# Optimization experiments

Hardware: AMD Instinct MI355X
Metric: run time of the kernel (lower is better)

Reference implementation:

```python
import jax, jax.numpy as jnp
import numpy as np

B, T, Q, K, H = 8, 128, 64, 64, 4  # batch, agents, q_dim, kv_dim, heads; neighbors n = T-1


def setup_inputs() -> dict:
    key = jax.random.key(0)
    ks = jax.random.split(key, 9)
    s = 0.05
    return {
        "q_x": jax.random.normal(ks[0], (B, T, Q), dtype=jnp.float32),
        "kv_x": jax.random.normal(ks[1], (B, T, T - 1, K), dtype=jnp.float32),
        # nn.Linear weights stored (out_features, in_features), y = x @ W.T + b
        "Wk": jax.random.normal(ks[2], (H * K, K), dtype=jnp.float32) * s,      # tokeys (no bias)
        "Wq": jax.random.normal(ks[3], (H * K, Q), dtype=jnp.float32) * s,      # toqueries (no bias)
        "Wv": jax.random.normal(ks[4], (H * K, K + Q), dtype=jnp.float32) * s,  # tovalues
        "bv": jax.random.normal(ks[5], (H * K,), dtype=jnp.float32) * s,
        "bias": jax.random.uniform(ks[6], (K,), dtype=jnp.float32, minval=-0.1, maxval=0.1),
        "ws": jax.random.normal(ks[7], (K,), dtype=jnp.float32) * s,            # score_proj weight (1, K) -> (K,)
        "bs": jax.random.normal(ks[8], (), dtype=jnp.float32) * s,              # score_proj bias
    }


def reference(q_x, kv_x, Wk, Wq, Wv, bv, bias, ws, bs):
    b, t, n, k = kv_x.shape            # n = t - 1 neighbors
    q = q_x.shape[-1]
    h = Wk.shape[0] // k
    # key / query projections
    keys = jnp.einsum('btnk,ok->btno', kv_x, Wk).reshape(b, t, n, h, k)
    queries = jnp.einsum('btq,oq->bto', q_x, Wq).reshape(b, t, 1, h, k)
    # additive (Bahdanau) score: linear(tanh(keys + queries + bias)) -> scalar per (b,t,n,h)
    score = jnp.einsum('btnhk,k->btnh', jnp.tanh(keys + queries + bias), ws) + bs
    # values from concat(kv, broadcast query features)
    q_exp = jnp.broadcast_to(q_x[:, :, None, :], (b, t, n, q))
    value_input = jnp.concatenate([kv_x, q_exp], axis=-1)      # (b,t,n,k+q)
    values = (jnp.einsum('btnc,oc->btno', value_input, Wv) + bv).reshape(b, t, n, h, k)
    # softmax over neighbors, weighted sum of values
    w = jax.nn.softmax(score, axis=2)                          # (b,t,n,h)
    x = jnp.einsum('btnh,btnhk->bthk', w, values).reshape(b, t, h * k)
    return x
```

## Files before the change

kernel.cpp:

```cpp
#include <hip/hip_runtime.h>
#include <hip/hip_bf16.h>

#define NB 127
#define SCALE 2.885390081777927f

typedef __attribute__((ext_vector_type(8))) short bf16x8;
typedef __attribute__((ext_vector_type(4))) float f32x4;

#define WKP_S  0
#define WVP_S  16384
#define WQP_S  32768
#define WVQP_S 49152
#define WS_NEEDED ((size_t)(4 * 16384 * 2))

__device__ __forceinline__ short bfs(float f) {
  __hip_bfloat16 h = __float2bfloat16(f);
  return __builtin_bit_cast(short, h);
}
__device__ __forceinline__ unsigned packbf2(float a, float b) {
  unsigned lo = (unsigned short)bfs(a);
  unsigned hi = (unsigned short)bfs(b);
  return lo | (hi << 16);
}
__device__ __forceinline__ float b2f(short s) {
  unsigned u = ((unsigned)(unsigned short)s) << 16;
  return __builtin_bit_cast(float, u);
}
__device__ __forceinline__ bf16x8 gath_s(const float* __restrict__ p, float s) {
  float4 a = *(const float4*)p;
  float4 b = *(const float4*)(p + 4);
  bf16x8 f;
  f[0] = bfs(a.x * s); f[1] = bfs(a.y * s); f[2] = bfs(a.z * s); f[3] = bfs(a.w * s);
  f[4] = bfs(b.x * s); f[5] = bfs(b.y * s); f[6] = bfs(b.z * s); f[7] = bfs(b.w * s);
  return f;
}

__global__ __launch_bounds__(256, 2) void
pack_kernel(const float* __restrict__ Wk, const float* __restrict__ Wq,
            const float* __restrict__ Wv, short* __restrict__ dstall)
{
  const int blk = blockIdx.x;
  const int tid = threadIdx.x;
  const int m = blk >> 4, sub = blk & 15;
  const float* src; int stride, off, dsto; float scl;
  if (m == 0)      { src = Wk; stride = 64;  off = 0;  dsto = WKP_S;  scl = SCALE; }
  else if (m == 1) { src = Wv; stride = 128; off = 0;  dsto = WVP_S;  scl = 1.f; }
  else if (m == 2) { src = Wq; stride = 64;  off = 0;  dsto = WQP_S;  scl = SCALE; }
  else             { src = Wv; stride = 128; off = 64; dsto = WVQP_S; scl = 1.f; }
  short* dst = dstall + dsto;
  int i4 = sub * 256 + tid;
  int o = i4 >> 4, c4 = i4 & 15;
  float4 v = ((const float4*)(src + o * stride + off))[c4];
  int k0 = c4 * 4;
  int kt = k0 >> 5, gg = (k0 & 31) >> 3, j0 = k0 & 7;
  int head = o >> 6, nt = (o >> 4) & 3, ol = o & 15;
  int di = ((((head * 4 + nt) * 2 + kt) * 64) + gg * 16 + ol) * 8 + j0;
  *(uint2*)(dst + di) = make_uint2(packbf2(v.x * scl, v.y * scl),
                                   packbf2(v.z * scl, v.w * scl));
}

template <int PREP>
__global__ __launch_bounds__(256, 4) void
rnn_attn_kernel(const float* __restrict__ q_x, const float* __restrict__ kv_x,
                const float* __restrict__ Wk, const float* __restrict__ Wq,
                const float* __restrict__ Wv, const float* __restrict__ bv,
                const float* __restrict__ bias, const float* __restrict__ wsc,
                const short* __restrict__ pack, float* __restrict__ out)
{
  __shared__ __align__(16) unsigned char Atile[128 * 128];
  __shared__ float scs[4][128];
  __shared__ float4 qv_lds[4][4][4];

  const int tid = threadIdx.x;
  const int bt = blockIdx.x;
  const int lane = tid & 63;
  const int head = tid >> 6;
  const int l15 = lane & 15;
  const int g = lane >> 4;

  const float* kv = kv_x + (size_t)bt * (NB * 64);
  #pragma unroll
  for (int i = 0; i < 8; ++i) {
    int idx = i * 256 + tid;
    int row = idx >> 4, c = idx & 15;
    float4 v = (row < NB) ? ((const float4*)kv)[idx] : make_float4(0.f, 0.f, 0.f, 0.f);
    int byte = (row << 7) + (c << 3);
    byte ^= ((row & 7) << 4);
    *(uint2*)(&Atile[byte]) = make_uint2(packbf2(v.x, v.y), packbf2(v.z, v.w));
  }

  f32x4 qq[4];
  {
    bf16x8 qf0 = gath_s(q_x + bt * 64 + g * 8, 1.f);
    bf16x8 qf1 = gath_s(q_x + bt * 64 + 32 + g * 8, 1.f);
    #pragma unroll
    for (int nt = 0; nt < 4; ++nt) {
      bf16x8 wv0, wv1;
      if (PREP) {
        const bf16x8* pv = (const bf16x8*)(pack + WVQP_S);
        wv0 = pv[((head * 4 + nt) * 2 + 0) * 64 + lane];
        wv1 = pv[((head * 4 + nt) * 2 + 1) * 64 + lane];
      } else {
        int o = head * 64 + nt * 16 + l15;
        wv0 = gath_s(Wv + o * 128 + 64 + g * 8, 1.f);
        wv1 = gath_s(Wv + o * 128 + 64 + 32 + g * 8, 1.f);
      }
      float4 bv4 = ((const float4*)(bv + head * 64))[nt * 4 + g];
      f32x4 b = (f32x4){bv4.x, bv4.y, bv4.z, bv4.w};
      b = __builtin_amdgcn_mfma_f32_16x16x32_bf16(wv0, qf0, b, 0, 0, 0);
      b = __builtin_amdgcn_mfma_f32_16x16x32_bf16(wv1, qf1, b, 0, 0, 0);
      if (l15 == 0) qv_lds[head][nt][g] = make_float4(b[0], b[1], b[2], b[3]);
    }
    #pragma unroll
    for (int nt = 0; nt < 4; ++nt) {
      bf16x8 wq0, wq1;
      if (PREP) {
        const bf16x8* pw = (const bf16x8*)(pack + WQP_S);
        wq0 = pw[((head * 4 + nt) * 2 + 0) * 64 + lane];
        wq1 = pw[((head * 4 + nt) * 2 + 1) * 64 + lane];
      } else {
        int o = head * 64 + nt * 16 + l15;
        wq0 = gath_s(Wq + o * 64 + g * 8, SCALE);
        wq1 = gath_s(Wq + o * 64 + 32 + g * 8, SCALE);
      }
      float4 bs4 = ((const float4*)bias)[nt * 4 + g];
      f32x4 a = (f32x4){bs4.x * SCALE, bs4.y * SCALE, bs4.z * SCALE, bs4.w * SCALE};
      a = __builtin_amdgcn_mfma_f32_16x16x32_bf16(wq0, qf0, a, 0, 0, 0);
      a = __builtin_amdgcn_mfma_f32_16x16x32_bf16(wq1, qf1, a, 0, 0, 0);
      qq[nt] = a;
    }
  }

  __syncthreads();

  #pragma unroll
  for (int h = 0; h < 2; ++h) {
    bf16x8 b00, b01, b10, b11;
    if (PREP) {
      const bf16x8* pw = (const bf16x8*)(pack + WKP_S);
      b00 = pw[((head * 4 + 2 * h + 0) * 2 + 0) * 64 + lane];
      b01 = pw[((head * 4 + 2 * h + 0) * 2 + 1) * 64 + lane];
      b10 = pw[((head * 4 + 2 * h + 1) * 2 + 0) * 64 + lane];
      b11 = pw[((head * 4 + 2 * h + 1) * 2 + 1) * 64 + lane];
    } else {
      int o0 = head * 64 + (2 * h) * 16 + l15;
      b00 = gath_s(Wk + o0 * 64 + g * 8, SCALE);
      b01 = gath_s(Wk + o0 * 64 + 32 + g * 8, SCALE);
      b10 = gath_s(Wk + (o0 + 16) * 64 + g * 8, SCALE);
      b11 = gath_s(Wk + (o0 + 16) * 64 + 32 + g * 8, SCALE);
    }
    float4 ta = ((const float4*)wsc)[(2 * h) * 4 + g];
    float4 tb = ((const float4*)wsc)[(2 * h + 1) * 4 + g];
    f32x4 wsa = (f32x4){-2.f * ta.x, -2.f * ta.y, -2.f * ta.z, -2.f * ta.w};
    f32x4 wsb = (f32x4){-2.f * tb.x, -2.f * tb.y, -2.f * tb.z, -2.f * tb.w};
    f32x4 qa = qq[2 * h], qb = qq[2 * h + 1];

    #pragma unroll 1
    for (int mt = 0; mt < 8; ++mt) {
      int row = mt * 16 + l15;
      int byte0 = (row << 7) + g * 16;
      int swz = (l15 & 7) << 4;
      bf16x8 a0 = *(const bf16x8*)(&Atile[byte0 ^ swz]);
      bf16x8 a1 = *(const bf16x8*)(&Atile[(byte0 + 64) ^ swz]);
      float p = 0.f;
      f32x4 acc = qa;
      acc = __builtin_amdgcn_mfma_f32_16x16x32_bf16(b00, a0, acc, 0, 0, 0);
      acc = __builtin_amdgcn_mfma_f32_16x16x32_bf16(b01, a1, acc, 0, 0, 0);
      #pragma unroll
      for (int r = 0; r < 4; ++r)
        p = fmaf(wsa[r], __builtin_amdgcn_rcpf(__builtin_amdgcn_exp2f(acc[r]) + 1.f), p);
      f32x4 acc2 = qb;
      acc2 = __builtin_amdgcn_mfma_f32_16x16x32_bf16(b10, a0, acc2, 0, 0, 0);
      acc2 = __builtin_amdgcn_mfma_f32_16x16x32_bf16(b11, a1, acc2, 0, 0, 0);
      #pragma unroll
      for (int r = 0; r < 4; ++r)
        p = fmaf(wsb[r], __builtin_amdgcn_rcpf(__builtin_amdgcn_exp2f(acc2[r]) + 1.f), p);
      p += __shfl_xor(p, 16);
      p += __shfl_xor(p, 32);
      if (g == 0) {
        int idx = mt * 16 + l15;
        scs[head][idx] = h ? (scs[head][idx] + p) : p;
      }
    }
  }

  {
    float s0 = scs[head][l15 + 0],  s1 = scs[head][l15 + 16];
    float s2 = scs[head][l15 + 32], s3 = scs[head][l15 + 48];
    float s4 = scs[head][l15 + 64], s5 = scs[head][l15 + 80];
    float s6 = scs[head][l15 + 96], s7 = scs[head][l15 + 112];
    if (l15 == 15) s7 = -3.0e38f;
    float m = fmaxf(fmaxf(fmaxf(s0, s1), fmaxf(s2, s3)),
                    fmaxf(fmaxf(s4, s5), fmaxf(s6, s7)));
    #pragma unroll
    for (int d = 1; d < 16; d <<= 1) m = fmaxf(m, __shfl_xor(m, d));
    float e0 = __expf(s0 - m), e1 = __expf(s1 - m), e2 = __expf(s2 - m), e3 = __expf(s3 - m);
    float e4 = __expf(s4 - m), e5 = __expf(s5 - m), e6 = __expf(s6 - m), e7 = __expf(s7 - m);
    float sum = ((e0 + e1) + (e2 + e3)) + ((e4 + e5) + (e6 + e7));
    #pragma unroll
    for (int d = 1; d < 16; d <<= 1) sum += __shfl_xor(sum, d);
    float inv = __builtin_amdgcn_rcpf(sum);
    if (g == 0) {
      scs[head][l15 + 0]  = e0 * inv; scs[head][l15 + 16] = e1 * inv;
      scs[head][l15 + 32] = e2 * inv; scs[head][l15 + 48] = e3 * inv;
      scs[head][l15 + 64] = e4 * inv; scs[head][l15 + 80] = e5 * inv;
      scs[head][l15 + 96] = e6 * inv; scs[head][l15 + 112] = e7 * inv;
    }
  }

  float pvp0[8], pvp1[8];
  #pragma unroll
  for (int j = 0; j < 8; ++j) { pvp0[j] = 0.f; pvp1[j] = 0.f; }
  #pragma unroll 1
  for (int mt = 0; mt < 8; ++mt) {
    int row = mt * 16 + l15;
    int byte0 = (row << 7) + g * 16;
    int swz = (l15 & 7) << 4;
    bf16x8 a0 = *(const bf16x8*)(&Atile[byte0 ^ swz]);
    bf16x8 a1 = *(const bf16x8*)(&Atile[(byte0 + 64) ^ swz]);
    float w = scs[head][mt * 16 + l15];
    #pragma unroll
    for (int j = 0; j < 8; ++j) {
      pvp0[j] = fmaf(w, b2f(a0[j]), pvp0[j]);
      pvp1[j] = fmaf(w, b2f(a1[j]), pvp1[j]);
    }
  }
  bf16x8 pa0, pa1;
  #pragma unroll
  for (int j = 0; j < 8; ++j) { pa0[j] = bfs(pvp0[j]); pa1[j] = bfs(pvp1[j]); }

  float tt[4];
  #pragma unroll 2
  for (int nt = 0; nt < 4; ++nt) {
    bf16x8 bw0, bw1;
    if (PREP) {
      const bf16x8* pw = (const bf16x8*)(pack + WVP_S);
      bw0 = pw[((head * 4 + nt) * 2 + 0) * 64 + lane];
      bw1 = pw[((head * 4 + nt) * 2 + 1) * 64 + lane];
    } else {
      int o = head * 64 + nt * 16 + l15;
      bw0 = gath_s(Wv + o * 128 + g * 8, 1.f);
      bw1 = gath_s(Wv + o * 128 + 32 + g * 8, 1.f);
    }
    f32x4 c = (f32x4){0.f, 0.f, 0.f, 0.f};
    c = __builtin_amdgcn_mfma_f32_16x16x32_bf16(pa0, bw0, c, 0, 0, 0);
    c = __builtin_amdgcn_mfma_f32_16x16x32_bf16(pa1, bw1, c, 0, 0, 0);
    float t = (c[0] + c[1]) + (c[2] + c[3]);
    t += __shfl_xor(t, 16);
    t += __shfl_xor(t, 32);
    tt[nt] = t;
  }

  float v = tt[0];
  v = (g == 1) ? tt[1] : v;
  v = (g == 2) ? tt[2] : v;
  v = (g == 3) ? tt[3] : v;
  float qv = ((const float*)&qv_lds[head][g][l15 >> 2])[l15 & 3];
  out[bt * 256 + head * 64 + lane] = v + qv;
}

extern "C" void kernel_launch(void* const* d_in, const int* in_sizes, int n_in,
                              void* d_out, int out_size, void* d_ws, size_t ws_size,
                              hipStream_t stream) {
  const float* q_x  = (const float*)d_in[0];
  const float* kv_x = (const float*)d_in[1];
  const float* Wk   = (const float*)d_in[2];
  const float* Wq   = (const float*)d_in[3];
  const float* Wv   = (const float*)d_in[4];
  const float* bv   = (const float*)d_in[5];
  const float* bias = (const float*)d_in[6];
  const float* wsc  = (const float*)d_in[7];
  float* out = (float*)d_out;
  short* pack = (short*)d_ws;

  if (ws_size >= WS_NEEDED) {
    pack_kernel<<<64, 256, 0, stream>>>(Wk, Wq, Wv, pack);
    rnn_attn_kernel<1><<<1024, 256, 0, stream>>>(q_x, kv_x, Wk, Wq, Wv, bv, bias, wsc, pack, out);
  } else {
    rnn_attn_kernel<0><<<1024, 256, 0, stream>>>(q_x, kv_x, Wk, Wq, Wv, bv, bias, wsc, pack, out);
  }
}
```

Before: 29.07 us.

## Process two (b,t) rows per block with a double-size kv tile

Each block now loads the kv tiles for two consecutive (b,t) rows into a doubled shared-memory buffer up front, then processes the two rows sequentially, and the grid is halved. The goal is more outstanding global loads per block and amortised block launch and setup cost. In exchange, LDS use per block roughly doubles, which lowers occupancy, and the second row's compute no longer overlaps with another block's loads. The scs and qv_lds buffers are reused across the two rows with no barrier between them. That is safe only because each wave touches only its own head slice.

```diff
diff --git a/kernel.cpp b/kernel.cpp
--- a/kernel.cpp
+++ b/kernel.cpp
@@ -67,196 +67,202 @@
                 const float* __restrict__ bias, const float* __restrict__ wsc,
                 const short* __restrict__ pack, float* __restrict__ out)
 {
-  __shared__ __align__(16) unsigned char Atile[128 * 128];
+  __shared__ __align__(16) unsigned char Atile[2][128 * 128];
   __shared__ float scs[4][128];
   __shared__ float4 qv_lds[4][4][4];
 
   const int tid = threadIdx.x;
-  const int bt = blockIdx.x;
+  const int bt0 = blockIdx.x * 2;
   const int lane = tid & 63;
   const int head = tid >> 6;
   const int l15 = lane & 15;
   const int g = lane >> 4;
 
-  const float* kv = kv_x + (size_t)bt * (NB * 64);
   #pragma unroll
-  for (int i = 0; i < 8; ++i) {
+  for (int i = 0; i < 16; ++i) {
     int idx = i * 256 + tid;
-    int row = idx >> 4, c = idx & 15;
-    float4 v = (row < NB) ? ((const float4*)kv)[idx] : make_float4(0.f, 0.f, 0.f, 0.f);
-    int byte = (row << 7) + (c << 3);
-    byte ^= ((row & 7) << 4);
-    *(uint2*)(&Atile[byte]) = make_uint2(packbf2(v.x, v.y), packbf2(v.z, v.w));
+    int tb = idx >> 11;
+    int id2 = idx & 2047;
+    int row = id2 >> 4, c = id2 & 15;
+    const float* kv = kv_x + (size_t)(bt0 + tb) * (NB * 64);
+    float4 v = (row < NB) ? ((const float4*)kv)[id2] : make_float4(0.f, 0.f, 0.f, 0.f);
+    int byte = (tb << 14) + ((((row << 7) + (c << 3))) ^ ((row & 7) << 4));
+    *(uint2*)(&Atile[0][0] + byte) = make_uint2(packbf2(v.x, v.y), packbf2(v.z, v.w));
   }
-
-  f32x4 qq[4];
-  {
-    bf16x8 qf0 = gath_s(q_x + bt * 64 + g * 8, 1.f);
-    bf16x8 qf1 = gath_s(q_x + bt * 64 + 32 + g * 8, 1.f);
+  __syncthreads();
+
+  #pragma unroll 1
+  for (int b = 0; b < 2; ++b) {
+    const int bt = bt0 + b;
+    const int tbase = b << 14;
+
+    f32x4 qq[4];
+    {
+      bf16x8 qf0 = gath_s(q_x + bt * 64 + g * 8, 1.f);
+      bf16x8 qf1 = gath_s(q_x + bt * 64 + 32 + g * 8, 1.f);
+      #pragma unroll
+      for (int nt = 0; nt < 4; ++nt) {
+        bf16x8 wv0, wv1;
+        if (PREP) {
+          const bf16x8* pv = (const bf16x8*)(pack + WVQP_S);
+          wv0 = pv[((head * 4 + nt) * 2 + 0) * 64 + lane];
+          wv1 = pv[((head * 4 + nt) * 2 + 1) * 64 + lane];
+        } else {
+          int o = head * 64 + nt * 16 + l15;
+          wv0 = gath_s(Wv + o * 128 + 64 + g * 8, 1.f);
+          wv1 = gath_s(Wv + o * 128 + 64 + 32 + g * 8, 1.f);
+        }
+        float4 bv4 = ((const float4*)(bv + head * 64))[nt * 4 + g];
+        f32x4 bb = (f32x4){bv4.x, bv4.y, bv4.z, bv4.w};
+        bb = __builtin_amdgcn_mfma_f32_16x16x32_bf16(wv0, qf0, bb, 0, 0, 0);
+        bb = __builtin_amdgcn_mfma_f32_16x16x32_bf16(wv1, qf1, bb, 0, 0, 0);
+        if (l15 == 0) qv_lds[head][nt][g] = make_float4(bb[0], bb[1], bb[2], bb[3]);
+      }
+      #pragma unroll
+      for (int nt = 0; nt < 4; ++nt) {
+        bf16x8 wq0, wq1;
+        if (PREP) {
+          const bf16x8* pw = (const bf16x8*)(pack + WQP_S);
+          wq0 = pw[((head * 4 + nt) * 2 + 0) * 64 + lane];
+          wq1 = pw[((head * 4 + nt) * 2 + 1) * 64 + lane];
+        } else {
+          int o = head * 64 + nt * 16 + l15;
+          wq0 = gath_s(Wq + o * 64 + g * 8, SCALE);
+          wq1 = gath_s(Wq + o * 64 + 32 + g * 8, SCALE);
+        }
+        float4 bs4 = ((const float4*)bias)[nt * 4 + g];
+        f32x4 a = (f32x4){bs4.x * SCALE, bs4.y * SCALE, bs4.z * SCALE, bs4.w * SCALE};
+        a = __builtin_amdgcn_mfma_f32_16x16x32_bf16(wq0, qf0, a, 0, 0, 0);
+        a = __builtin_amdgcn_mfma_f32_16x16x32_bf16(wq1, qf1, a, 0, 0, 0);
+        qq[nt] = a;
+      }
+    }
+
     #pragma unroll
-    for (int nt = 0; nt < 4; ++nt) {
-      bf16x8 wv0, wv1;
+    for (int h = 0; h < 2; ++h) {
+      bf16x8 b00, b01, b10, b11;
       if (PREP) {
-        const bf16x8* pv = (const bf16x8*)(pack + WVQP_S);
-        wv0 = pv[((head * 4 + nt) * 2 + 0) * 64 + lane];
-        wv1 = pv[((head * 4 + nt) * 2 + 1) * 64 + lane];
+        const bf16x8* pw = (const bf16x8*)(pack + WKP_S);
+        b00 = pw[((head * 4 + 2 * h + 0) * 2 + 0) * 64 + lane];
+        b01 = pw[((head * 4 + 2 * h + 0) * 2 + 1) * 64 + lane];
+        b10 = pw[((head * 4 + 2 * h + 1) * 2 + 0) * 64 + lane];
+        b11 = pw[((head * 4 + 2 * h + 1) * 2 + 1) * 64 + lane];
       } else {
-        int o = head * 64 + nt * 16 + l15;
-        wv0 = gath_s(Wv + o * 128 + 64 + g * 8, 1.f);
-        wv1 = gath_s(Wv + o * 128 + 64 + 32 + g * 8, 1.f);
-      }
-      float4 bv4 = ((const float4*)(bv + head * 64))[nt * 4 + g];
-      f32x4 b = (f32x4){bv4.x, bv4.y, bv4.z, bv4.w};
-      b = __builtin_amdgcn_mfma_f32_16x16x32_bf16(wv0, qf0, b, 0, 0, 0);
-      b = __builtin_amdgcn_mfma_f32_16x16x32_bf16(wv1, qf1, b, 0, 0, 0);
-      if (l15 == 0) qv_lds[head][nt][g] = make_float4(b[0], b[1], b[2], b[3]);
-    }
+        int o0 = head * 64 + (2 * h) * 16 + l15;
+        b00 = gath_s(Wk + o0 * 64 + g * 8, SCALE);
+        b01 = gath_s(Wk + o0 * 64 + 32 + g * 8, SCALE);
+        b10 = gath_s(Wk + (o0 + 16) * 64 + g * 8, SCALE);
+        b11 = gath_s(Wk + (o0 + 16) * 64 + 32 + g * 8, SCALE);
+      }
+      float4 ta = ((const float4*)wsc)[(2 * h) * 4 + g];
+      float4 tb = ((const float4*)wsc)[(2 * h + 1) * 4 + g];
+      f32x4 wsa = (f32x4){-2.f * ta.x, -2.f * ta.y, -2.f * ta.z, -2.f * ta.w};
+      f32x4 wsb = (f32x4){-2.f * tb.x, -2.f * tb.y, -2.f * tb.z, -2.f * tb.w};
+      f32x4 qa = qq[2 * h], qb = qq[2 * h + 1];
+
+      #pragma unroll 1
+      for (int mt = 0; mt < 8; ++mt) {
+        int row = mt * 16 + l15;
+        int byte0 = tbase + (row << 7) + g * 16;
+        int swz = (l15 & 7) << 4;
+        bf16x8 a0 = *(const bf16x8*)(&Atile[0][0] + (byte0 ^ swz));
+        bf16x8 a1 = *(const bf16x8*)(&Atile[0][0] + ((byte0 + 64) ^ swz));
+        float p = 0.f;
+        f32x4 acc = qa;
+        acc = __builtin_amdgcn_mfma_f32_16x16x32_bf16(b00, a0, acc, 0, 0, 0);
+        acc = __builtin_amdgcn_mfma_f32_16x16x32_bf16(b01, a1, acc, 0, 0, 0);
+        #pragma unroll
+        for (int r = 0; r < 4; ++r)
+          p = fmaf(wsa[r], __builtin_amdgcn_rcpf(__builtin_amdgcn_exp2f(acc[r]) + 1.f), p);
+        f32x4 acc2 = qb;
+        acc2 = __builtin_amdgcn_mfma_f32_16x16x32_bf16(b10, a0, acc2, 0, 0, 0);
+        acc2 = __builtin_amdgcn_mfma_f32_16x16x32_bf16(b11, a1, acc2, 0, 0, 0);
+        #pragma unroll
+        for (int r = 0; r < 4; ++r)
+          p = fmaf(wsb[r], __builtin_amdgcn_rcpf(__builtin_amdgcn_exp2f(acc2[r]) + 1.f), p);
+        p += __shfl_xor(p, 16);
+        p += __shfl_xor(p, 32);
+        if (g == 0) {
+          int idx = mt * 16 + l15;
+          scs[head][idx] = h ? (scs[head][idx] + p) : p;
+        }
+      }
+    }
+
+    {
+      float s0 = scs[head][l15 + 0],  s1 = scs[head][l15 + 16];
+      float s2 = scs[head][l15 + 32], s3 = scs[head][l15 + 48];
+      float s4 = scs[head][l15 + 64], s5 = scs[head][l15 + 80];
+      float s6 = scs[head][l15 + 96], s7 = scs[head][l15 + 112];
+      if (l15 == 15) s7 = -3.0e38f;
+      float m = fmaxf(fmaxf(fmaxf(s0, s1), fmaxf(s2, s3)),
+                      fmaxf(fmaxf(s4, s5), fmaxf(s6, s7)));
+      #pragma unroll
+      for (int d = 1; d < 16; d <<= 1) m = fmaxf(m, __shfl_xor(m, d));
+      float e0 = __expf(s0 - m), e1 = __expf(s1 - m), e2 = __expf(s2 - m), e3 = __expf(s3 - m);
+      float e4 = __expf(s4 - m), e5 = __expf(s5 - m), e6 = __expf(s6 - m), e7 = __expf(s7 - m);
+      float sum = ((e0 + e1) + (e2 + e3)) + ((e4 + e5) + (e6 + e7));
+      #pragma unroll
+      for (int d = 1; d < 16; d <<= 1) sum += __shfl_xor(sum, d);
+      float inv = __builtin_amdgcn_rcpf(sum);
+      if (g == 0) {
+        scs[head][l15 + 0]  = e0 * inv; scs[head][l15 + 16] = e1 * inv;
+        scs[head][l15 + 32] = e2 * inv; scs[head][l15 + 48] = e3 * inv;
+        scs[head][l15 + 64] = e4 * inv; scs[head][l15 + 80] = e5 * inv;
+        scs[head][l15 + 96] = e6 * inv; scs[head][l15 + 112] = e7 * inv;
+      }
+    }
+
+    float pvp0[8], pvp1[8];
     #pragma unroll
-    for (int nt = 0; nt < 4; ++nt) {
-      bf16x8 wq0, wq1;
-      if (PREP) {
-        const bf16x8* pw = (const bf16x8*)(pack + WQP_S);
-        wq0 = pw[((head * 4 + nt) * 2 + 0) * 64 + lane];
-        wq1 = pw[((head * 4 + nt) * 2 + 1) * 64 + lane];
-      } else {
-        int o = head * 64 + nt * 16 + l15;
-        wq0 = gath_s(Wq + o * 64 + g * 8, SCALE);
-        wq1 = gath_s(Wq + o * 64 + 32 + g * 8, SCALE);
-      }
-      float4 bs4 = ((const float4*)bias)[nt * 4 + g];
-      f32x4 a = (f32x4){bs4.x * SCALE, bs4.y * SCALE, bs4.z * SCALE, bs4.w * SCALE};
-      a = __builtin_amdgcn_mfma_f32_16x16x32_bf16(wq0, qf0, a, 0, 0, 0);
-      a = __builtin_amdgcn_mfma_f32_16x16x32_bf16(wq1, qf1, a, 0, 0, 0);
-      qq[nt] = a;
-    }
-  }
-
-  __syncthreads();
-
-  #pragma unroll
-  for (int h = 0; h < 2; ++h) {
-    bf16x8 b00, b01, b10, b11;
-    if (PREP) {
-      const bf16x8* pw = (const bf16x8*)(pack + WKP_S);
-      b00 = pw[((head * 4 + 2 * h + 0) * 2 + 0) * 64 + lane];
-      b01 = pw[((head * 4 + 2 * h + 0) * 2 + 1) * 64 + lane];
-      b10 = pw[((head * 4 + 2 * h + 1) * 2 + 0) * 64 + lane];
-      b11 = pw[((head * 4 + 2 * h + 1) * 2 + 1) * 64 + lane];
-    } else {
-      int o0 = head * 64 + (2 * h) * 16 + l15;
-      b00 = gath_s(Wk + o0 * 64 + g * 8, SCALE);
-      b01 = gath_s(Wk + o0 * 64 + 32 + g * 8, SCALE);
-      b10 = gath_s(Wk + (o0 + 16) * 64 + g * 8, SCALE);
-      b11 = gath_s(Wk + (o0 + 16) * 64 + 32 + g * 8, SCALE);
-    }
-    float4 ta = ((const float4*)wsc)[(2 * h) * 4 + g];
-    float4 tb = ((const float4*)wsc)[(2 * h + 1) * 4 + g];
-    f32x4 wsa = (f32x4){-2.f * ta.x, -2.f * ta.y, -2.f * ta.z, -2.f * ta.w};
-    f32x4 wsb = (f32x4){-2.f * tb.x, -2.f * tb.y, -2.f * tb.z, -2.f * tb.w};
-    f32x4 qa = qq[2 * h], qb = qq[2 * h + 1];
-
+    for (int j = 0; j < 8; ++j) { pvp0[j] = 0.f; pvp1[j] = 0.f; }
     #pragma unroll 1
     for (int mt = 0; mt < 8; ++mt) {
       int row = mt * 16 + l15;
-      int byte0 = (row << 7) + g * 16;
+      int byte0 = tbase + (row << 7) + g * 16;
       int swz = (l15 & 7) << 4;
-      bf16x8 a0 = *(const bf16x8*)(&Atile[byte0 ^ swz]);
-      bf16x8 a1 = *(const bf16x8*)(&Atile[(byte0 + 64) ^ swz]);
-      float p = 0.f;
-      f32x4 acc = qa;
-      acc = __builtin_amdgcn_mfma_f32_16x16x32_bf16(b00, a0, acc, 0, 0, 0);
-      acc = __builtin_amdgcn_mfma_f32_16x16x32_bf16(b01, a1, acc, 0, 0, 0);
-      #pragma unroll
-      for (int r = 0; r < 4; ++r)
-        p = fmaf(wsa[r], __builtin_amdgcn_rcpf(__builtin_amdgcn_exp2f(acc[r]) + 1.f), p);
-      f32x4 acc2 = qb;
-      acc2 = __builtin_amdgcn_mfma_f32_16x16x32_bf16(b10, a0, acc2, 0, 0, 0);
-      acc2 = __builtin_amdgcn_mfma_f32_16x16x32_bf16(b11, a1, acc2, 0, 0, 0);
-      #pragma unroll
-      for (int r = 0; r < 4; ++r)
-        p = fmaf(wsb[r], __builtin_amdgcn_rcpf(__builtin_amdgcn_exp2f(acc2[r]) + 1.f), p);
-      p += __shfl_xor(p, 16);
-      p += __shfl_xor(p, 32);
-      if (g == 0) {
-        int idx = mt * 16 + l15;
-        scs[head][idx] = h ? (scs[head][idx] + p) : p;
-      }
-    }
+      bf16x8 a0 = *(const bf16x8*)(&Atile[0][0] + (byte0 ^ swz));
+      bf16x8 a1 = *(const bf16x8*)(&Atile[0][0] + ((byte0 + 64) ^ swz));
+      float w = scs[head][mt * 16 + l15];
+      #pragma unroll
+      for (int j = 0; j < 8; ++j) {
+        pvp0[j] = fmaf(w, b2f(a0[j]), pvp0[j]);
+        pvp1[j] = fmaf(w, b2f(a1[j]), pvp1[j]);
+      }
+    }
+    bf16x8 pa0, pa1;
+    #pragma unroll
+    for (int j = 0; j < 8; ++j) { pa0[j] = bfs(pvp0[j]); pa1[j] = bfs(pvp1[j]); }
+
+    float tt[4];
+    #pragma unroll 2
+    for (int nt = 0; nt < 4; ++nt) {
+      bf16x8 bw0, bw1;
+      if (PREP) {
+        const bf16x8* pw = (const bf16x8*)(pack + WVP_S);
+        bw0 = pw[((head * 4 + nt) * 2 + 0) * 64 + lane];
+        bw1 = pw[((head * 4 + nt) * 2 + 1) * 64 + lane];
+      } else {
+        int o = head * 64 + nt * 16 + l15;
+        bw0 = gath_s(Wv + o * 128 + g * 8, 1.f);
+        bw1 = gath_s(Wv + o * 128 + 32 + g * 8, 1.f);
+      }
+      f32x4 c = (f32x4){0.f, 0.f, 0.f, 0.f};
+      c = __builtin_amdgcn_mfma_f32_16x16x32_bf16(pa0, bw0, c, 0, 0, 0);
+      c = __builtin_amdgcn_mfma_f32_16x16x32_bf16(pa1, bw1, c, 0, 0, 0);
+      float t = (c[0] + c[1]) + (c[2] + c[3]);
+      t += __shfl_xor(t, 16);
+      t += __shfl_xor(t, 32);
+      tt[nt] = t;
+    }
+
+    float v = tt[0];
+    v = (g == 1) ? tt[1] : v;
+    v = (g == 2) ? tt[2] : v;
+    v = (g == 3) ? tt[3] : v;
+    float qv = ((const float*)&qv_lds[head][g][l15 >> 2])[l15 & 3];
+    out[bt * 256 + head * 64 + lane] = v + qv;
   }
-
-  {
-    float s0 = scs[head][l15 + 0],  s1 = scs[head][l15 + 16];
-    float s2 = scs[head][l15 + 32], s3 = scs[head][l15 + 48];
-    float s4 = scs[head][l15 + 64], s5 = scs[head][l15 + 80];
-    float s6 = scs[head][l15 + 96], s7 = scs[head][l15 + 112];
-    if (l15 == 15) s7 = -3.0e38f;
-    float m = fmaxf(fmaxf(fmaxf(s0, s1), fmaxf(s2, s3)),
-                    fmaxf(fmaxf(s4, s5), fmaxf(s6, s7)));
-    #pragma unroll
-    for (int d = 1; d < 16; d <<= 1) m = fmaxf(m, __shfl_xor(m, d));
-    float e0 = __expf(s0 - m), e1 = __expf(s1 - m), e2 = __expf(s2 - m), e3 = __expf(s3 - m);
-    float e4 = __expf(s4 - m), e5 = __expf(s5 - m), e6 = __expf(s6 - m), e7 = __expf(s7 - m);
-    float sum = ((e0 + e1) + (e2 + e3)) + ((e4 + e5) + (e6 + e7));
-    #pragma unroll
-    for (int d = 1; d < 16; d <<= 1) sum += __shfl_xor(sum, d);
-    float inv = __builtin_amdgcn_rcpf(sum);
-    if (g == 0) {
-      scs[head][l15 + 0]  = e0 * inv; scs[head][l15 + 16] = e1 * inv;
-      scs[head][l15 + 32] = e2 * inv; scs[head][l15 + 48] = e3 * inv;
-      scs[head][l15 + 64] = e4 * inv; scs[head][l15 + 80] = e5 * inv;
-      scs[head][l15 + 96] = e6 * inv; scs[head][l15 + 112] = e7 * inv;
-    }
-  }
-
-  float pvp0[8], pvp1[8];
-  #pragma unroll
-  for (int j = 0; j < 8; ++j) { pvp0[j] = 0.f; pvp1[j] = 0.f; }
-  #pragma unroll 1
-  for (int mt = 0; mt < 8; ++mt) {
-    int row = mt * 16 + l15;
-    int byte0 = (row << 7) + g * 16;
-    int swz = (l15 & 7) << 4;
-    bf16x8 a0 = *(const bf16x8*)(&Atile[byte0 ^ swz]);
-    bf16x8 a1 = *(const bf16x8*)(&Atile[(byte0 + 64) ^ swz]);
-    float w = scs[head][mt * 16 + l15];
-    #pragma unroll
-    for (int j = 0; j < 8; ++j) {
-      pvp0[j] = fmaf(w, b2f(a0[j]), pvp0[j]);
-      pvp1[j] = fmaf(w, b2f(a1[j]), pvp1[j]);
-    }
-  }
-  bf16x8 pa0, pa1;
-  #pragma unroll
-  for (int j = 0; j < 8; ++j) { pa0[j] = bfs(pvp0[j]); pa1[j] = bfs(pvp1[j]); }
-
-  float tt[4];
-  #pragma unroll 2
-  for (int nt = 0; nt < 4; ++nt) {
-    bf16x8 bw0, bw1;
-    if (PREP) {
-      const bf16x8* pw = (const bf16x8*)(pack + WVP_S);
-      bw0 = pw[((head * 4 + nt) * 2 + 0) * 64 + lane];
-      bw1 = pw[((head * 4 + nt) * 2 + 1) * 64 + lane];
-    } else {
-      int o = head * 64 + nt * 16 + l15;
-      bw0 = gath_s(Wv + o * 128 + g * 8, 1.f);
-      bw1 = gath_s(Wv + o * 128 + 32 + g * 8, 1.f);
-    }
-    f32x4 c = (f32x4){0.f, 0.f, 0.f, 0.f};
-    c = __builtin_amdgcn_mfma_f32_16x16x32_bf16(pa0, bw0, c, 0, 0, 0);
-    c = __builtin_amdgcn_mfma_f32_16x16x32_bf16(pa1, bw1, c, 0, 0, 0);
-    float t = (c[0] + c[1]) + (c[2] + c[3]);
-    t += __shfl_xor(t, 16);
-    t += __shfl_xor(t, 32);
-    tt[nt] = t;
-  }
-
-  float v = tt[0];
-  v = (g == 1) ? tt[1] : v;
-  v = (g == 2) ? tt[2] : v;
-  v = (g == 3) ? tt[3] : v;
-  float qv = ((const float*)&qv_lds[head][g][l15 >> 2])[l15 & 3];
-  out[bt * 256 + head * 64 + lane] = v + qv;
 }
 
 extern "C" void kernel_launch(void* const* d_in, const int* in_sizes, int n_in,
@@ -275,8 +281,8 @@
 
   if (ws_size >= WS_NEEDED) {
     pack_kernel<<<64, 256, 0, stream>>>(Wk, Wq, Wv, pack);
-    rnn_attn_kernel<1><<<1024, 256, 0, stream>>>(q_x, kv_x, Wk, Wq, Wv, bv, bias, wsc, pack, out);
+    rnn_attn_kernel<1><<<512, 256, 0, stream>>>(q_x, kv_x, Wk, Wq, Wv, bv, bias, wsc, pack, out);
   } else {
-    rnn_attn_kernel<0><<<1024, 256, 0, stream>>>(q_x, kv_x, Wk, Wq, Wv, bv, bias, wsc, pack, out);
+    rnn_attn_kernel<0><<<512, 256, 0, stream>>>(q_x, kv_x, Wk, Wq, Wv, bv, bias, wsc, pack, out);
   }
 }
```

Result: slower. 53.15 us (+82.8%).

## Split each (b,t) block into two head-pair blocks with neighbor halves per wave

Applied to the files above, without the earlier changes.

The grid doubles to 2048 blocks, each handling two heads for one (b,t). Two waves per head each process half of the 128 neighbor rows. Partial scores meet in LDS behind an extra barrier, and the two halves' PV outputs are summed through LDS before the store. Launch bounds rise to 6 blocks per CU. The aim is more parallelism and occupancy, at the cost of each block reloading and converting the full kv tile (twice the global reads of kv_x), plus extra syncs.

```diff
diff --git a/kernel.cpp b/kernel.cpp
--- a/kernel.cpp
+++ b/kernel.cpp
@@ -60,7 +60,7 @@
 }
 
 template <int PREP>
-__global__ __launch_bounds__(256, 4) void
+__global__ __launch_bounds__(256, 6) void
 rnn_attn_kernel(const float* __restrict__ q_x, const float* __restrict__ kv_x,
                 const float* __restrict__ Wk, const float* __restrict__ Wq,
                 const float* __restrict__ Wv, const float* __restrict__ bv,
@@ -68,13 +68,19 @@
                 const short* __restrict__ pack, float* __restrict__ out)
 {
   __shared__ __align__(16) unsigned char Atile[128 * 128];
-  __shared__ float scs[4][128];
-  __shared__ float4 qv_lds[4][4][4];
+  __shared__ float scs[2][128];
+  __shared__ float ps[4][64];
+  __shared__ float4 qv_lds[2][4][4];
 
   const int tid = threadIdx.x;
-  const int bt = blockIdx.x;
+  const int blk = blockIdx.x;
+  const int bt = blk & 1023;
+  const int hp = blk >> 10;
   const int lane = tid & 63;
-  const int head = tid >> 6;
+  const int wv = tid >> 6;
+  const int head_l = wv >> 1;
+  const int half = wv & 1;
+  const int head = hp * 2 + head_l;
   const int l15 = lane & 15;
   const int g = lane >> 4;
 
@@ -93,25 +99,27 @@
   {
     bf16x8 qf0 = gath_s(q_x + bt * 64 + g * 8, 1.f);
     bf16x8 qf1 = gath_s(q_x + bt * 64 + 32 + g * 8, 1.f);
-    #pragma unroll
-    for (int nt = 0; nt < 4; ++nt) {
-      bf16x8 wv0, wv1;
-      if (PREP) {
-        const bf16x8* pv = (const bf16x8*)(pack + WVQP_S);
-        wv0 = pv[((head * 4 + nt) * 2 + 0) * 64 + lane];
-        wv1 = pv[((head * 4 + nt) * 2 + 1) * 64 + lane];
-      } else {
-        int o = head * 64 + nt * 16 + l15;
-        wv0 = gath_s(Wv + o * 128 + 64 + g * 8, 1.f);
-        wv1 = gath_s(Wv + o * 128 + 64 + 32 + g * 8, 1.f);
+    if (half == 0) {
+      #pragma unroll 2
+      for (int nt = 0; nt < 4; ++nt) {
+        bf16x8 wv0, wv1;
+        if (PREP) {
+          const bf16x8* pv = (const bf16x8*)(pack + WVQP_S);
+          wv0 = pv[((head * 4 + nt) * 2 + 0) * 64 + lane];
+          wv1 = pv[((head * 4 + nt) * 2 + 1) * 64 + lane];
+        } else {
+          int o = head * 64 + nt * 16 + l15;
+          wv0 = gath_s(Wv + o * 128 + 64 + g * 8, 1.f);
+          wv1 = gath_s(Wv + o * 128 + 64 + 32 + g * 8, 1.f);
+        }
+        float4 bv4 = ((const float4*)(bv + head * 64))[nt * 4 + g];
+        f32x4 b = (f32x4){bv4.x, bv4.y, bv4.z, bv4.w};
+        b = __builtin_amdgcn_mfma_f32_16x16x32_bf16(wv0, qf0, b, 0, 0, 0);
+        b = __builtin_amdgcn_mfma_f32_16x16x32_bf16(wv1, qf1, b, 0, 0, 0);
+        if (l15 == 0) qv_lds[head_l][nt][g] = make_float4(b[0], b[1], b[2], b[3]);
       }
-      float4 bv4 = ((const float4*)(bv + head * 64))[nt * 4 + g];
-      f32x4 b = (f32x4){bv4.x, bv4.y, bv4.z, bv4.w};
-      b = __builtin_amdgcn_mfma_f32_16x16x32_bf16(wv0, qf0, b, 0, 0, 0);
-      b = __builtin_amdgcn_mfma_f32_16x16x32_bf16(wv1, qf1, b, 0, 0, 0);
-      if (l15 == 0) qv_lds[head][nt][g] = make_float4(b[0], b[1], b[2], b[3]);
-    }
-    #pragma unroll
+    }
+    #pragma unroll 2
     for (int nt = 0; nt < 4; ++nt) {
       bf16x8 wq0, wq1;
       if (PREP) {
@@ -133,7 +141,7 @@
 
   __syncthreads();
 
-  #pragma unroll
+  #pragma unroll 1
   for (int h = 0; h < 2; ++h) {
     bf16x8 b00, b01, b10, b11;
     if (PREP) {
@@ -156,8 +164,8 @@
     f32x4 qa = qq[2 * h], qb = qq[2 * h + 1];
 
     #pragma unroll 1
-    for (int mt = 0; mt < 8; ++mt) {
-      int row = mt * 16 + l15;
+    for (int mt = 0; mt < 4; ++mt) {
+      int row = half * 64 + mt * 16 + l15;
       int byte0 = (row << 7) + g * 16;
       int swz = (l15 & 7) << 4;
       bf16x8 a0 = *(const bf16x8*)(&Atile[byte0 ^ swz]);
@@ -178,17 +186,20 @@
       p += __shfl_xor(p, 16);
       p += __shfl_xor(p, 32);
       if (g == 0) {
-        int idx = mt * 16 + l15;
-        scs[head][idx] = h ? (scs[head][idx] + p) : p;
+        int idx = half * 64 + mt * 16 + l15;
+        scs[head_l][idx] = h ? (scs[head_l][idx] + p) : p;
       }
     }
   }
 
+  __syncthreads();
+
+  float w0, w1, w2, w3;
   {
-    float s0 = scs[head][l15 + 0],  s1 = scs[head][l15 + 16];
-    float s2 = scs[head][l15 + 32], s3 = scs[head][l15 + 48];
-    float s4 = scs[head][l15 + 64], s5 = scs[head][l15 + 80];
-    float s6 = scs[head][l15 + 96], s7 = scs[head][l15 + 112];
+    float s0 = scs[head_l][l15 + 0],  s1 = scs[head_l][l15 + 16];
+    float s2 = scs[head_l][l15 + 32], s3 = scs[head_l][l15 + 48];
+    float s4 = scs[head_l][l15 + 64], s5 = scs[head_l][l15 + 80];
+    float s6 = scs[head_l][l15 + 96], s7 = scs[head_l][l15 + 112];
     if (l15 == 15) s7 = -3.0e38f;
     float m = fmaxf(fmaxf(fmaxf(s0, s1), fmaxf(s2, s3)),
                     fmaxf(fmaxf(s4, s5), fmaxf(s6, s7)));
@@ -200,25 +211,21 @@
     #pragma unroll
     for (int d = 1; d < 16; d <<= 1) sum += __shfl_xor(sum, d);
     float inv = __builtin_amdgcn_rcpf(sum);
-    if (g == 0) {
-      scs[head][l15 + 0]  = e0 * inv; scs[head][l15 + 16] = e1 * inv;
-      scs[head][l15 + 32] = e2 * inv; scs[head][l15 + 48] = e3 * inv;
-      scs[head][l15 + 64] = e4 * inv; scs[head][l15 + 80] = e5 * inv;
-      scs[head][l15 + 96] = e6 * inv; scs[head][l15 + 112] = e7 * inv;
-    }
+    if (half) { w0 = e4 * inv; w1 = e5 * inv; w2 = e6 * inv; w3 = e7 * inv; }
+    else      { w0 = e0 * inv; w1 = e1 * inv; w2 = e2 * inv; w3 = e3 * inv; }
   }
 
   float pvp0[8], pvp1[8];
   #pragma unroll
   for (int j = 0; j < 8; ++j) { pvp0[j] = 0.f; pvp1[j] = 0.f; }
   #pragma unroll 1
-  for (int mt = 0; mt < 8; ++mt) {
-    int row = mt * 16 + l15;
+  for (int mt = 0; mt < 4; ++mt) {
+    int row = half * 64 + mt * 16 + l15;
     int byte0 = (row << 7) + g * 16;
     int swz = (l15 & 7) << 4;
     bf16x8 a0 = *(const bf16x8*)(&Atile[byte0 ^ swz]);
     bf16x8 a1 = *(const bf16x8*)(&Atile[(byte0 + 64) ^ swz]);
-    float w = scs[head][mt * 16 + l15];
+    float w = (mt == 0) ? w0 : (mt == 1) ? w1 : (mt == 2) ? w2 : w3;
     #pragma unroll
     for (int j = 0; j < 8; ++j) {
       pvp0[j] = fmaf(w, b2f(a0[j]), pvp0[j]);
@@ -229,8 +236,7 @@
   #pragma unroll
   for (int j = 0; j < 8; ++j) { pa0[j] = bfs(pvp0[j]); pa1[j] = bfs(pvp1[j]); }
 
-  float tt[4];
-  #pragma unroll 2
+  #pragma unroll 1
   for (int nt = 0; nt < 4; ++nt) {
     bf16x8 bw0, bw1;
     if (PREP) {
@@ -248,15 +254,16 @@
     float t = (c[0] + c[1]) + (c[2] + c[3]);
     t += __shfl_xor(t, 16);
     t += __shfl_xor(t, 32);
-    tt[nt] = t;
-  }
-
-  float v = tt[0];
-  v = (g == 1) ? tt[1] : v;
-  v = (g == 2) ? tt[2] : v;
-  v = (g == 3) ? tt[3] : v;
-  float qv = ((const float*)&qv_lds[head][g][l15 >> 2])[l15 & 3];
-  out[bt * 256 + head * 64 + lane] = v + qv;
+    if (g == 0) ps[wv][nt * 16 + l15] = t;
+  }
+
+  __syncthreads();
+
+  if (half == 0) {
+    float v = ps[wv][lane] + ps[wv + 1][lane];
+    float qv = ((const float*)&qv_lds[head_l][lane >> 4][(lane & 15) >> 2])[lane & 3];
+    out[bt * 256 + head * 64 + lane] = v + qv;
+  }
 }
 
 extern "C" void kernel_launch(void* const* d_in, const int* in_sizes, int n_in,
@@ -275,8 +282,8 @@
 
   if (ws_size >= WS_NEEDED) {
     pack_kernel<<<64, 256, 0, stream>>>(Wk, Wq, Wv, pack);
-    rnn_attn_kernel<1><<<1024, 256, 0, stream>>>(q_x, kv_x, Wk, Wq, Wv, bv, bias, wsc, pack, out);
+    rnn_attn_kernel<1><<<2048, 256, 0, stream>>>(q_x, kv_x, Wk, Wq, Wv, bv, bias, wsc, pack, out);
   } else {
-    rnn_attn_kernel<0><<<1024, 256, 0, stream>>>(q_x, kv_x, Wk, Wq, Wv, bv, bias, wsc, pack, out);
-  }
-}
+    rnn_attn_kernel<0><<<2048, 256, 0, stream>>>(q_x, kv_x, Wk, Wq, Wv, bv, bias, wsc, pack, out);
+  }
+}
```

Result: slower. 34.31 us (+18.0%).
